# Kernel optimization log

Hardware: AMD Instinct MI355X
Metric: run time of the kernel (lower is better)

The kernel has to match this reference:

```python
import jax, jax.numpy as jnp
import numpy as np

N_NODES = 100000


def sage_conv(x, src, dst, W_l, b_l, W_r):
    # PyG SAGEConv (aggr='mean'): out = lin_l(mean_{j->i} x_j) + lin_r(x_i)
    # lin_l has bias, lin_r does not.
    msgs = x[src]                                             # [E, d_in] irregular gather
    summed = jax.ops.segment_sum(msgs, dst, num_segments=N_NODES)
    deg = jax.ops.segment_sum(jnp.ones((src.shape[0],), x.dtype), dst,
                              num_segments=N_NODES)
    mean = summed / jnp.maximum(deg, 1.0)[:, None]            # [N, d_in]
    return mean @ W_l.T + b_l + x @ W_r.T                     # [N, d_out]


def setup_inputs() -> dict:
    key = jax.random.key(0)
    ks = jax.random.split(key, 8)
    input_dim, hidden_dim, output_dim = 64, 128, 64
    E = 1600000
    x = jax.random.normal(ks[0], (N_NODES, input_dim), dtype=jnp.float32)
    edge_index = jax.random.randint(ks[1], (2, E), 0, N_NODES, dtype=jnp.int64)

    def glorot(k, shape):
        lim = (6.0 / (shape[0] + shape[1])) ** 0.5
        return jax.random.uniform(k, shape, jnp.float32, -lim, lim)

    W1_l = glorot(ks[2], (hidden_dim, input_dim))
    b1 = jnp.zeros((hidden_dim,), jnp.float32)
    W1_r = glorot(ks[3], (hidden_dim, input_dim))
    W2_l = glorot(ks[4], (output_dim, hidden_dim))
    b2 = jnp.zeros((output_dim,), jnp.float32)
    W2_r = glorot(ks[5], (output_dim, hidden_dim))
    return {"x": x, "edge_index": edge_index,
            "W1_l": W1_l, "b1": b1, "W1_r": W1_r,
            "W2_l": W2_l, "b2": b2, "W2_r": W2_r}


def reference(x, edge_index, W1_l, b1, W1_r, W2_l, b2, W2_r):
    src, dst = edge_index[0], edge_index[1]
    h = jax.nn.relu(sage_conv(x, src, dst, W1_l, b1, W1_r))
    h = jax.nn.relu(sage_conv(h, src, dst, W2_l, b2, W2_r))
    # Original module computes norm(x) and dropout(x) but discards the results,
    # so the returned value is just the second ReLU output.
    return h
```

## Files before the change

### kernel.cpp

```cpp
#include <hip/hip_runtime.h>
#include <hip/hip_bf16.h>


#define NODE_DIM0 64
#define NPBK 512
#define MAXB 256
#define CAPB 12288
#define EPB  4096

__device__ inline unsigned short f2bf(float f) {
    unsigned u = __float_as_uint(f);
    return (unsigned short)((u + 0x7fffu + ((u >> 16) & 1u)) >> 16);
}


__global__ __launch_bounds__(256) void bucket_scatter(const int* __restrict__ src,
                                                      const int* __restrict__ dst,
                                                      int* __restrict__ gcur,
                                                      unsigned* __restrict__ pairs, int E) {
    __shared__ int hist[MAXB];
    __shared__ int incl[MAXB];
    __shared__ int exoff[MAXB];
    __shared__ int cur[MAXB];
    __shared__ int chunkBase[MAXB];
    __shared__ unsigned staged[EPB];
    __shared__ unsigned char sbkt[EPB];
    const int t = threadIdx.x;
    const int base = blockIdx.x * EPB;
    int cnt = E - base; if (cnt > EPB) cnt = EPB;

    hist[t] = 0;
    __syncthreads();

    int myS[16], myD[16];
#pragma unroll
    for (int it = 0; it < 16; ++it) {
        int e = base + it * 256 + t;
        if (e < E) {
            myS[it] = src[e];
            myD[it] = dst[e];
            atomicAdd(&hist[myD[it] >> 9], 1);
        } else {
            myD[it] = -1;
        }
    }
    __syncthreads();

    incl[t] = hist[t];
    __syncthreads();
    for (int o = 1; o < 256; o <<= 1) {
        int add = (t >= o) ? incl[t - o] : 0;
        __syncthreads();
        incl[t] += add;
        __syncthreads();
    }
    exoff[t] = incl[t] - hist[t];
    cur[t] = 0;
    chunkBase[t] = (hist[t] > 0) ? atomicAdd(&gcur[t], hist[t]) : 0;
    __syncthreads();

#pragma unroll
    for (int it = 0; it < 16; ++it) {
        if (myD[it] >= 0) {
            int b = myD[it] >> 9;
            int p = exoff[b] + atomicAdd(&cur[b], 1);
            staged[p] = ((unsigned)(myD[it] & (NPBK - 1)) << 17) | (unsigned)myS[it];
            sbkt[p] = (unsigned char)b;
        }
    }
    __syncthreads();

    for (int p = t; p < cnt; p += 256) {
        int b = sbkt[p];
        int g = chunkBase[b] + (p - exoff[b]);
        if (g < CAPB) pairs[(size_t)b * CAPB + g] = staged[p];
    }
}


__global__ __launch_bounds__(256) void bucket_csr(const unsigned* __restrict__ pairs,
                                                  const int* __restrict__ gcur,
                                                  int* __restrict__ startA,
                                                  int* __restrict__ degA,
                                                  int* __restrict__ esrc, int N) {
    __shared__ int ldeg[NPBK];
    __shared__ int scn[NPBK];
    __shared__ int lcur[NPBK];
    __shared__ int lsrc[CAPB];
    const int b = blockIdx.x;
    const int t = threadIdx.x;
    const int node0 = b * NPBK;
    int cnt = gcur[b]; if (cnt > CAPB) cnt = CAPB;

    ldeg[t] = 0; ldeg[t + 256] = 0;
    __syncthreads();

    const unsigned* reg = pairs + (size_t)b * CAPB;
    for (int i = t; i < cnt; i += 256)
        atomicAdd(&ldeg[reg[i] >> 17], 1);
    __syncthreads();

    scn[t] = ldeg[t]; scn[t + 256] = ldeg[t + 256];
    __syncthreads();
    for (int o = 1; o < NPBK; o <<= 1) {
        int a0 = (t >= o) ? scn[t - o] : 0;
        int a1 = (t + 256 >= o) ? scn[t + 256 - o] : 0;
        __syncthreads();
        scn[t] += a0; scn[t + 256] += a1;
        __syncthreads();
    }
    int e0 = scn[t] - ldeg[t];
    int e1 = scn[t + 256] - ldeg[t + 256];
    lcur[t] = e0; lcur[t + 256] = e1;
    const int gbase = b * CAPB;
    if (node0 + t < N)       { startA[node0 + t] = gbase + e0;       degA[node0 + t] = ldeg[t]; }
    if (node0 + 256 + t < N) { startA[node0 + 256 + t] = gbase + e1; degA[node0 + 256 + t] = ldeg[t + 256]; }
    __syncthreads();

    for (int i = t; i < cnt; i += 256) {
        unsigned w = reg[i];
        int pos = atomicAdd(&lcur[w >> 17], 1);
        lsrc[pos] = (int)(w & 0x1FFFFu);
    }
    __syncthreads();

    int* out = esrc + (size_t)b * CAPB;
    for (int i = t; i < cnt; i += 256) out[i] = lsrc[i];
}


__global__ void cast_bf(const float* __restrict__ in, unsigned short* __restrict__ out, int n4) {
    int i = blockIdx.x * 256 + threadIdx.x;
    if (i < n4) {
        float4 v = ((const float4*)in)[i];
        ushort4 o;
        o.x = f2bf(v.x); o.y = f2bf(v.y); o.z = f2bf(v.z); o.w = f2bf(v.w);
        ((ushort4*)out)[i] = o;
    }
}

__global__ void cast_weights(const float* __restrict__ a, const float* __restrict__ b,
                             const float* __restrict__ c, const float* __restrict__ d,
                             unsigned short* __restrict__ oa, unsigned short* __restrict__ ob,
                             unsigned short* __restrict__ oc, unsigned short* __restrict__ od) {
    int i = blockIdx.x * 256 + threadIdx.x;
    if (i < 8192) {
        oa[i] = f2bf(a[i]); ob[i] = f2bf(b[i]);
        oc[i] = f2bf(c[i]); od[i] = f2bf(d[i]);
    }
}


template <int MODE>
__global__ __launch_bounds__(256) void gather64(const unsigned short* __restrict__ feat,
                                                const int* __restrict__ startA,
                                                const int* __restrict__ degA,
                                                const int* __restrict__ esrc,
                                                const unsigned short* __restrict__ sdata,
                                                unsigned short* __restrict__ meanOut,
                                                float* __restrict__ outF, int n) {
    int w = blockIdx.x * 4 + (threadIdx.x >> 6);
    int lane = threadIdx.x & 63;
    if (w >= n) return;
    int s0 = startA[w], dg = degA[w];
    int s1 = s0 + dg;
    int grp = lane >> 3;
    int fl  = lane & 7;
    float acc[8] = {0.f, 0.f, 0.f, 0.f, 0.f, 0.f, 0.f, 0.f};
    for (int base = s0; base < s1; base += 64) {
        int sv = (base + lane < s1) ? esrc[base + lane] : 0;
        int cnt = s1 - base; if (cnt > 64) cnt = 64;
        int sidx[8];
#pragma unroll
        for (int k = 0; k < 8; ++k)
            sidx[k] = __shfl(sv, grp + 8 * k);
        uint4 u[8];
#pragma unroll
        for (int k = 0; k < 8; ++k)
            if (grp + 8 * k < cnt)
                u[k] = *(const uint4*)(feat + (size_t)sidx[k] * 64 + fl * 8);
#pragma unroll
        for (int k = 0; k < 8; ++k) {
            if (grp + 8 * k < cnt) {
                acc[0] += __uint_as_float(u[k].x << 16);
                acc[1] += __uint_as_float(u[k].x & 0xffff0000u);
                acc[2] += __uint_as_float(u[k].y << 16);
                acc[3] += __uint_as_float(u[k].y & 0xffff0000u);
                acc[4] += __uint_as_float(u[k].z << 16);
                acc[5] += __uint_as_float(u[k].z & 0xffff0000u);
                acc[6] += __uint_as_float(u[k].w << 16);
                acc[7] += __uint_as_float(u[k].w & 0xffff0000u);
            }
        }
    }
#pragma unroll
    for (int o = 8; o < 64; o <<= 1) {
#pragma unroll
        for (int q = 0; q < 8; ++q) acc[q] += __shfl_xor(acc[q], o);
    }
    if (lane < 8) {
        float inv = 1.0f / fmaxf((float)dg, 1.0f);
        if (MODE == 0) {
            unsigned us[8];
#pragma unroll
            for (int q = 0; q < 8; ++q) us[q] = f2bf(acc[q] * inv);
            uint4 o4;
            o4.x = us[0] | (us[1] << 16);
            o4.y = us[2] | (us[3] << 16);
            o4.z = us[4] | (us[5] << 16);
            o4.w = us[6] | (us[7] << 16);
            *(uint4*)(meanOut + (size_t)w * 64 + fl * 8) = o4;
        } else {
            uint4 us = *(const uint4*)(sdata + (size_t)w * 64 + fl * 8);
            float sv8[8];
            sv8[0] = __uint_as_float(us.x << 16);
            sv8[1] = __uint_as_float(us.x & 0xffff0000u);
            sv8[2] = __uint_as_float(us.y << 16);
            sv8[3] = __uint_as_float(us.y & 0xffff0000u);
            sv8[4] = __uint_as_float(us.z << 16);
            sv8[5] = __uint_as_float(us.z & 0xffff0000u);
            sv8[6] = __uint_as_float(us.w << 16);
            sv8[7] = __uint_as_float(us.w & 0xffff0000u);
            float4 o0, o1;
            o0.x = fmaxf(acc[0] * inv + sv8[0], 0.f);
            o0.y = fmaxf(acc[1] * inv + sv8[1], 0.f);
            o0.z = fmaxf(acc[2] * inv + sv8[2], 0.f);
            o0.w = fmaxf(acc[3] * inv + sv8[3], 0.f);
            o1.x = fmaxf(acc[4] * inv + sv8[4], 0.f);
            o1.y = fmaxf(acc[5] * inv + sv8[5], 0.f);
            o1.z = fmaxf(acc[6] * inv + sv8[6], 0.f);
            o1.w = fmaxf(acc[7] * inv + sv8[7], 0.f);
            *(float4*)(outF + (size_t)w * 64 + fl * 8)     = o0;
            *(float4*)(outF + (size_t)w * 64 + fl * 8 + 4) = o1;
        }
    }
}


template <int IN, int OUT, int NREP>
__global__ __launch_bounds__(256) void gemm_mfma(const unsigned short* __restrict__ meanb,
                                                 const unsigned short* __restrict__ selfb,
                                                 const unsigned short* __restrict__ Wl,
                                                 const float* __restrict__ bias,
                                                 const unsigned short* __restrict__ Wr,
                                                 unsigned short* __restrict__ outp, int n) {
    using bf16x8 = __attribute__((ext_vector_type(8))) short;
    using f32x4  = __attribute__((ext_vector_type(4))) float;
    constexpr int KK = IN / 32;
    constexpr int NT = OUT / 16;
    constexpr int NG = NT / NREP;
    const int wid  = blockIdx.x * 4 + (threadIdx.x >> 6);
    const int lane = threadIdx.x & 63;
    const int row16 = lane & 15;
    const int quad  = lane >> 4;
    const int ng  = wid % NG;
    const int mt0 = wid / NG;
    const int mstride = (gridDim.x * 4) / NG;
    const int mtiles = n / 16;

    bf16x8 bl[NREP][KK], br[NREP][KK];
    float bv[NREP];
#pragma unroll
    for (int r = 0; r < NREP; ++r) {
        int ncol = (ng * NREP + r) * 16 + row16;
#pragma unroll
        for (int kk = 0; kk < KK; ++kk) {
            bl[r][kk] = *(const bf16x8*)(Wl + (size_t)ncol * IN + kk * 32 + quad * 8);
            br[r][kk] = *(const bf16x8*)(Wr + (size_t)ncol * IN + kk * 32 + quad * 8);
        }
        bv[r] = bias[ncol];
    }

    for (int mt = mt0; mt < mtiles; mt += mstride) {
        const int m = mt * 16 + row16;
        bf16x8 am[KK], as2[KK];
#pragma unroll
        for (int kk = 0; kk < KK; ++kk) {
            am[kk]  = *(const bf16x8*)(meanb + (size_t)m * IN + kk * 32 + quad * 8);
            as2[kk] = *(const bf16x8*)(selfb + (size_t)m * IN + kk * 32 + quad * 8);
        }
#pragma unroll
        for (int r = 0; r < NREP; ++r) {
            f32x4 acc = {0.f, 0.f, 0.f, 0.f};
#pragma unroll
            for (int kk = 0; kk < KK; ++kk)
                acc = __builtin_amdgcn_mfma_f32_16x16x32_bf16(am[kk], bl[r][kk], acc, 0, 0, 0);
#pragma unroll
            for (int kk = 0; kk < KK; ++kk)
                acc = __builtin_amdgcn_mfma_f32_16x16x32_bf16(as2[kk], br[r][kk], acc, 0, 0, 0);
            const int ncol = (ng * NREP + r) * 16 + row16;
            const int rowb = mt * 16 + quad * 4;
#pragma unroll
            for (int i = 0; i < 4; ++i) {
                float v = fmaxf(acc[i] + bv[r], 0.f);
                outp[(size_t)(rowb + i) * OUT + ncol] = f2bf(v);
            }
        }
    }
}


template <int IN, int OUT, int NREP>
__global__ __launch_bounds__(256) void gemm_dual2(const unsigned short* __restrict__ A,
                                                  const unsigned short* __restrict__ Wl,
                                                  const float* __restrict__ bias,
                                                  const unsigned short* __restrict__ Wr,
                                                  unsigned short* __restrict__ zout,
                                                  unsigned short* __restrict__ sout, int n) {
    using bf16x8 = __attribute__((ext_vector_type(8))) short;
    using f32x4  = __attribute__((ext_vector_type(4))) float;
    constexpr int KK = IN / 32;
    constexpr int NT = OUT / 16;
    constexpr int NG = NT / NREP;
    const int wid  = blockIdx.x * 4 + (threadIdx.x >> 6);
    const int lane = threadIdx.x & 63;
    const int row16 = lane & 15;
    const int quad  = lane >> 4;
    const int ng  = wid % NG;
    const int mt0 = wid / NG;
    const int mstride = (gridDim.x * 4) / NG;
    const int mtiles = n / 16;

    bf16x8 bl[NREP][KK], br[NREP][KK];
    float bv[NREP];
#pragma unroll
    for (int r = 0; r < NREP; ++r) {
        int ncol = (ng * NREP + r) * 16 + row16;
#pragma unroll
        for (int kk = 0; kk < KK; ++kk) {
            bl[r][kk] = *(const bf16x8*)(Wl + (size_t)ncol * IN + kk * 32 + quad * 8);
            br[r][kk] = *(const bf16x8*)(Wr + (size_t)ncol * IN + kk * 32 + quad * 8);
        }
        bv[r] = bias[ncol];
    }

    for (int mt = mt0; mt < mtiles; mt += mstride) {
        const int m = mt * 16 + row16;
        bf16x8 am[KK];
#pragma unroll
        for (int kk = 0; kk < KK; ++kk)
            am[kk] = *(const bf16x8*)(A + (size_t)m * IN + kk * 32 + quad * 8);
#pragma unroll
        for (int r = 0; r < NREP; ++r) {
            f32x4 accz = {0.f, 0.f, 0.f, 0.f};
            f32x4 accs = {0.f, 0.f, 0.f, 0.f};
#pragma unroll
            for (int kk = 0; kk < KK; ++kk) {
                accz = __builtin_amdgcn_mfma_f32_16x16x32_bf16(am[kk], bl[r][kk], accz, 0, 0, 0);
                accs = __builtin_amdgcn_mfma_f32_16x16x32_bf16(am[kk], br[r][kk], accs, 0, 0, 0);
            }
            const int ncol = (ng * NREP + r) * 16 + row16;
            const int rowb = mt * 16 + quad * 4;
#pragma unroll
            for (int i = 0; i < 4; ++i) {
                zout[(size_t)(rowb + i) * OUT + ncol] = f2bf(accz[i]);
                sout[(size_t)(rowb + i) * OUT + ncol] = f2bf(accs[i] + bv[r]);
            }
        }
    }
}


static inline char* align_up(char* p, size_t a) {
    return (char*)(((uintptr_t)p + a - 1) & ~(uintptr_t)(a - 1));
}

extern "C" void kernel_launch(void* const* d_in, const int* in_sizes, int n_in,
                              void* d_out, int out_size, void* d_ws, size_t ws_size,
                              hipStream_t stream) {
    const float* x   = (const float*)d_in[0];
    const int*   ei  = (const int*)d_in[1];
    const float* W1l = (const float*)d_in[2];
    const float* b1  = (const float*)d_in[3];
    const float* W1r = (const float*)d_in[4];
    const float* W2l = (const float*)d_in[5];
    const float* b2  = (const float*)d_in[6];
    const float* W2r = (const float*)d_in[7];
    float* out = (float*)d_out;

    const int N = in_sizes[0] / NODE_DIM0;
    const int E = in_sizes[1] / 2;
    const int* src = ei;
    const int* dst = ei + E;
    const int nbuck = (N + NPBK - 1) / NPBK;

    char* p = (char*)d_ws;
    int* gcur   = (int*)p; p += (size_t)MAXB * 4;          p = align_up(p, 16);
    int* startA = (int*)p; p += (size_t)N * 4;             p = align_up(p, 16);
    int* degA   = (int*)p; p += (size_t)N * 4;             p = align_up(p, 16);
    int* esrc   = (int*)p; p += (size_t)nbuck * CAPB * 4;  p = align_up(p, 16);
    unsigned short* xbf   = (unsigned short*)p; p += (size_t)N * 64 * 2;
    unsigned short* h1bf  = (unsigned short*)p; p += (size_t)N * 128 * 2;
    unsigned short* scr2  = (unsigned short*)p; p += (size_t)N * 128 * 2;
    unsigned short* wl1bf = (unsigned short*)p; p += (size_t)128 * 64 * 2;
    unsigned short* wr1bf = (unsigned short*)p; p += (size_t)128 * 64 * 2;
    unsigned short* wl2bf = (unsigned short*)p; p += (size_t)64 * 128 * 2;
    unsigned short* wr2bf = (unsigned short*)p; p += (size_t)64 * 128 * 2;

    unsigned* pairs = (unsigned*)scr2;
    unsigned short* meanbf = scr2;
    unsigned short* zbf = scr2;
    unsigned short* sbf = scr2 + (size_t)N * 64;

    hipMemsetAsync(gcur, 0, (size_t)MAXB * 4, stream);
    bucket_scatter<<<(E + EPB - 1) / EPB, 256, 0, stream>>>(src, dst, gcur, pairs, E);
    bucket_csr<<<nbuck, 256, 0, stream>>>(pairs, gcur, startA, degA, esrc, N);

    cast_bf<<<(N * 64 / 4 + 255) / 256, 256, 0, stream>>>(x, xbf, N * 64 / 4);
    cast_weights<<<32, 256, 0, stream>>>(W1l, W1r, W2l, W2r, wl1bf, wr1bf, wl2bf, wr2bf);

    gather64<0><<<(N + 3) / 4, 256, 0, stream>>>(xbf, startA, degA, esrc, nullptr, meanbf, nullptr, N);
    gemm_mfma<64, 128, 2><<<512, 256, 0, stream>>>(meanbf, xbf, wl1bf, b1, wr1bf, h1bf, N);

    gemm_dual2<128, 64, 2><<<512, 256, 0, stream>>>(h1bf, wl2bf, b2, wr2bf, zbf, sbf, N);
    gather64<1><<<(N + 3) / 4, 256, 0, stream>>>(zbf, startA, degA, esrc, sbf, nullptr, out, N);
}
```

Measured before the change: 262.0 us.

## Assign eight lanes per node in gather instead of a full wavefront

The mean-aggregation gather now maps each destination node to an 8-lane group rather than a 64-lane wavefront, so one wavefront handles 8 nodes. Each group walks its own edge list with 4-way unrolled loads and no cross-lane shuffles or reductions. This removes the idle lanes and the shuffle reduction cost that come from nodes of average degree 16 occupying a whole wavefront. In exchange, loads are less parallel within a node and uneven degrees across the 8 nodes in a wavefront can cause divergence.

```diff
diff --git a/kernel.cpp b/kernel.cpp
--- a/kernel.cpp
+++ b/kernel.cpp
@@ -159,80 +159,77 @@
                                                 const unsigned short* __restrict__ sdata,
                                                 unsigned short* __restrict__ meanOut,
                                                 float* __restrict__ outF, int n) {
-    int w = blockIdx.x * 4 + (threadIdx.x >> 6);
-    int lane = threadIdx.x & 63;
+    const int w = (blockIdx.x * 256 + threadIdx.x) >> 3;
+    const int fl = threadIdx.x & 7;
     if (w >= n) return;
-    int s0 = startA[w], dg = degA[w];
-    int s1 = s0 + dg;
-    int grp = lane >> 3;
-    int fl  = lane & 7;
+    const int s0 = startA[w], dg = degA[w];
     float acc[8] = {0.f, 0.f, 0.f, 0.f, 0.f, 0.f, 0.f, 0.f};
-    for (int base = s0; base < s1; base += 64) {
-        int sv = (base + lane < s1) ? esrc[base + lane] : 0;
-        int cnt = s1 - base; if (cnt > 64) cnt = 64;
-        int sidx[8];
-#pragma unroll
-        for (int k = 0; k < 8; ++k)
-            sidx[k] = __shfl(sv, grp + 8 * k);
-        uint4 u[8];
-#pragma unroll
-        for (int k = 0; k < 8; ++k)
-            if (grp + 8 * k < cnt)
-                u[k] = *(const uint4*)(feat + (size_t)sidx[k] * 64 + fl * 8);
-#pragma unroll
-        for (int k = 0; k < 8; ++k) {
-            if (grp + 8 * k < cnt) {
-                acc[0] += __uint_as_float(u[k].x << 16);
-                acc[1] += __uint_as_float(u[k].x & 0xffff0000u);
-                acc[2] += __uint_as_float(u[k].y << 16);
-                acc[3] += __uint_as_float(u[k].y & 0xffff0000u);
-                acc[4] += __uint_as_float(u[k].z << 16);
-                acc[5] += __uint_as_float(u[k].z & 0xffff0000u);
-                acc[6] += __uint_as_float(u[k].w << 16);
-                acc[7] += __uint_as_float(u[k].w & 0xffff0000u);
-            }
-        }
-    }
-#pragma unroll
-    for (int o = 8; o < 64; o <<= 1) {
-#pragma unroll
-        for (int q = 0; q < 8; ++q) acc[q] += __shfl_xor(acc[q], o);
-    }
-    if (lane < 8) {
-        float inv = 1.0f / fmaxf((float)dg, 1.0f);
-        if (MODE == 0) {
-            unsigned us[8];
-#pragma unroll
-            for (int q = 0; q < 8; ++q) us[q] = f2bf(acc[q] * inv);
-            uint4 o4;
-            o4.x = us[0] | (us[1] << 16);
-            o4.y = us[2] | (us[3] << 16);
-            o4.z = us[4] | (us[5] << 16);
-            o4.w = us[6] | (us[7] << 16);
-            *(uint4*)(meanOut + (size_t)w * 64 + fl * 8) = o4;
-        } else {
-            uint4 us = *(const uint4*)(sdata + (size_t)w * 64 + fl * 8);
-            float sv8[8];
-            sv8[0] = __uint_as_float(us.x << 16);
-            sv8[1] = __uint_as_float(us.x & 0xffff0000u);
-            sv8[2] = __uint_as_float(us.y << 16);
-            sv8[3] = __uint_as_float(us.y & 0xffff0000u);
-            sv8[4] = __uint_as_float(us.z << 16);
-            sv8[5] = __uint_as_float(us.z & 0xffff0000u);
-            sv8[6] = __uint_as_float(us.w << 16);
-            sv8[7] = __uint_as_float(us.w & 0xffff0000u);
-            float4 o0, o1;
-            o0.x = fmaxf(acc[0] * inv + sv8[0], 0.f);
-            o0.y = fmaxf(acc[1] * inv + sv8[1], 0.f);
-            o0.z = fmaxf(acc[2] * inv + sv8[2], 0.f);
-            o0.w = fmaxf(acc[3] * inv + sv8[3], 0.f);
-            o1.x = fmaxf(acc[4] * inv + sv8[4], 0.f);
-            o1.y = fmaxf(acc[5] * inv + sv8[5], 0.f);
-            o1.z = fmaxf(acc[6] * inv + sv8[6], 0.f);
-            o1.w = fmaxf(acc[7] * inv + sv8[7], 0.f);
-            *(float4*)(outF + (size_t)w * 64 + fl * 8)     = o0;
-            *(float4*)(outF + (size_t)w * 64 + fl * 8 + 4) = o1;
-        }
+    const int* ep = esrc + s0;
+    int e = 0;
+    for (; e + 4 <= dg; e += 4) {
+        int s_[4];
+#pragma unroll
+        for (int k = 0; k < 4; ++k) s_[k] = ep[e + k];
+        uint4 u[4];
+#pragma unroll
+        for (int k = 0; k < 4; ++k)
+            u[k] = *(const uint4*)(feat + (size_t)s_[k] * 64 + fl * 8);
+#pragma unroll
+        for (int k = 0; k < 4; ++k) {
+            acc[0] += __uint_as_float(u[k].x << 16);
+            acc[1] += __uint_as_float(u[k].x & 0xffff0000u);
+            acc[2] += __uint_as_float(u[k].y << 16);
+            acc[3] += __uint_as_float(u[k].y & 0xffff0000u);
+            acc[4] += __uint_as_float(u[k].z << 16);
+            acc[5] += __uint_as_float(u[k].z & 0xffff0000u);
+            acc[6] += __uint_as_float(u[k].w << 16);
+            acc[7] += __uint_as_float(u[k].w & 0xffff0000u);
+        }
+    }
+    for (; e < dg; ++e) {
+        uint4 u = *(const uint4*)(feat + (size_t)ep[e] * 64 + fl * 8);
+        acc[0] += __uint_as_float(u.x << 16);
+        acc[1] += __uint_as_float(u.x & 0xffff0000u);
+        acc[2] += __uint_as_float(u.y << 16);
+        acc[3] += __uint_as_float(u.y & 0xffff0000u);
+        acc[4] += __uint_as_float(u.z << 16);
+        acc[5] += __uint_as_float(u.z & 0xffff0000u);
+        acc[6] += __uint_as_float(u.w << 16);
+        acc[7] += __uint_as_float(u.w & 0xffff0000u);
+    }
+    const float inv = 1.0f / fmaxf((float)dg, 1.0f);
+    if (MODE == 0) {
+        unsigned us[8];
+#pragma unroll
+        for (int q = 0; q < 8; ++q) us[q] = f2bf(acc[q] * inv);
+        uint4 o4;
+        o4.x = us[0] | (us[1] << 16);
+        o4.y = us[2] | (us[3] << 16);
+        o4.z = us[4] | (us[5] << 16);
+        o4.w = us[6] | (us[7] << 16);
+        *(uint4*)(meanOut + (size_t)w * 64 + fl * 8) = o4;
+    } else {
+        uint4 us = *(const uint4*)(sdata + (size_t)w * 64 + fl * 8);
+        float sv8[8];
+        sv8[0] = __uint_as_float(us.x << 16);
+        sv8[1] = __uint_as_float(us.x & 0xffff0000u);
+        sv8[2] = __uint_as_float(us.y << 16);
+        sv8[3] = __uint_as_float(us.y & 0xffff0000u);
+        sv8[4] = __uint_as_float(us.z << 16);
+        sv8[5] = __uint_as_float(us.z & 0xffff0000u);
+        sv8[6] = __uint_as_float(us.w << 16);
+        sv8[7] = __uint_as_float(us.w & 0xffff0000u);
+        float4 o0, o1;
+        o0.x = fmaxf(acc[0] * inv + sv8[0], 0.f);
+        o0.y = fmaxf(acc[1] * inv + sv8[1], 0.f);
+        o0.z = fmaxf(acc[2] * inv + sv8[2], 0.f);
+        o0.w = fmaxf(acc[3] * inv + sv8[3], 0.f);
+        o1.x = fmaxf(acc[4] * inv + sv8[4], 0.f);
+        o1.y = fmaxf(acc[5] * inv + sv8[5], 0.f);
+        o1.z = fmaxf(acc[6] * inv + sv8[6], 0.f);
+        o1.w = fmaxf(acc[7] * inv + sv8[7], 0.f);
+        *(float4*)(outF + (size_t)w * 64 + fl * 8)     = o0;
+        *(float4*)(outF + (size_t)w * 64 + fl * 8 + 4) = o1;
     }
 }
 
@@ -409,9 +406,9 @@
     cast_bf<<<(N * 64 / 4 + 255) / 256, 256, 0, stream>>>(x, xbf, N * 64 / 4);
     cast_weights<<<32, 256, 0, stream>>>(W1l, W1r, W2l, W2r, wl1bf, wr1bf, wl2bf, wr2bf);
 
-    gather64<0><<<(N + 3) / 4, 256, 0, stream>>>(xbf, startA, degA, esrc, nullptr, meanbf, nullptr, N);
+    gather64<0><<<(N * 8 + 255) / 256, 256, 0, stream>>>(xbf, startA, degA, esrc, nullptr, meanbf, nullptr, N);
     gemm_mfma<64, 128, 2><<<512, 256, 0, stream>>>(meanbf, xbf, wl1bf, b1, wr1bf, h1bf, N);
 
     gemm_dual2<128, 64, 2><<<512, 256, 0, stream>>>(h1bf, wl2bf, b2, wr2bf, zbf, sbf, N);
-    gather64<1><<<(N + 3) / 4, 256, 0, stream>>>(zbf, startA, degA, esrc, sbf, nullptr, out, N);
-}
+    gather64<1><<<(N * 8 + 255) / 256, 256, 0, stream>>>(zbf, startA, degA, esrc, sbf, nullptr, out, N);
+}
```

After: 228.9 us. 1.14x faster.
